# Performance work log

Measured on AMD Instinct MI355X. Metric: run time of the kernel, lower is better.

Reference implementation:

```python
import jax, jax.numpy as jnp
import numpy as np

N = 50000   # nodes
E = 600000  # edges
D = 128     # in_feats == n_hidden


def setup_inputs() -> dict:
    key = jax.random.key(0)
    ks = jax.random.split(key, 10)
    s = 0.1
    return {
        "x": jax.random.normal(ks[0], (N, D), jnp.float32),
        "W1": jax.random.normal(ks[1], (D, D), jnp.float32) * s,
        "b1": jnp.zeros((D,), jnp.float32),
        "W2": jax.random.normal(ks[2], (D, D), jnp.float32) * s,
        "b2": jnp.zeros((D,), jnp.float32),
        "Wp": jax.random.normal(ks[3], (D, D), jnp.float32) * s,
        "bp": jnp.zeros((D,), jnp.float32),
        "edge_src": jax.random.randint(ks[4], (E,), 0, N),
        "edge_dst": jax.random.randint(ks[5], (E,), 0, N),
        "perm": jax.random.randint(ks[6], (N,), 0, N),
    }


def _graph_conv(h, W, b, src, dst, norm):
    # DGL GraphConv (norm='both'): D^-1/2 A D^-1/2 H W + b
    m = h[src] * norm[src, None]                      # [E, D] gather
    agg = jax.ops.segment_sum(m, dst, num_segments=N)  # [N, D] scatter-add
    return (agg * norm[:, None]) @ W + b


def _encode(x, W1, b1, W2, b2, src, dst, norm):
    h = jax.nn.relu(_graph_conv(x, W1, b1, src, dst, norm))
    return _graph_conv(h, W2, b2, src, dst, norm)


def reference(x, W1, b1, W2, b2, Wp, bp, edge_src, edge_dst, perm):
    # symmetric normalization from in-degree (clamped to avoid div by 0)
    deg = jax.ops.segment_sum(jnp.ones((E,), x.dtype), edge_dst, num_segments=N)
    norm = jax.lax.rsqrt(jnp.maximum(deg, 1.0))

    h1 = _encode(x, W1, b1, W2, b2, edge_src, edge_dst, norm)        # clean
    h2 = _encode(x[perm], W1, b1, W2, b2, edge_src, edge_dst, norm)  # corrupt

    sc1 = (h1 @ Wp + bp).sum(axis=1)  # [N]
    sc2 = (h2 @ Wp + bp).sum(axis=1)  # [N]

    logits = jnp.concatenate([sc1, sc2])                   # [2N]
    lbl = jnp.concatenate([jnp.ones((N,), x.dtype), jnp.zeros((N,), x.dtype)])
    # BCEWithLogitsLoss (mean): softplus(z) - z*y  (numerically stable)
    loss = jnp.mean(jax.nn.softplus(logits) - logits * lbl)
    return loss
```

## Files before the change

kernel.cpp:

```cpp
#include <hip/hip_runtime.h>
#include <math.h>

#define D 128

typedef float f32x2 __attribute__((ext_vector_type(2)));
typedef float f32x4 __attribute__((ext_vector_type(4)));
typedef short short8 __attribute__((ext_vector_type(8)));

__device__ __forceinline__ float softplusf(float z){
    return log1pf(expf(-fabsf(z))) + fmaxf(z, 0.f);
}
__device__ __forceinline__ unsigned short f2bf(float f){
    unsigned u = __float_as_uint(f);
    u += 0x7fffu + ((u >> 16) & 1u);
    return (unsigned short)(u >> 16);
}
__device__ __forceinline__ int wt_idx(int row, int k){
    return row*128 + ((((k >> 3) ^ (row & 7)) << 3) | (k & 7));
}

__global__ void __launch_bounds__(256) k_fused1(
    const float* __restrict__ x, const float* __restrict__ W1,
    unsigned* __restrict__ xw8, int N,
    const int* __restrict__ edst, int* __restrict__ deg, int E,
    int nGemm,
    const float* __restrict__ W2, const float* __restrict__ b2,
    const float* __restrict__ Wp, const float* __restrict__ bp,
    float* __restrict__ v, float* __restrict__ cconst)
{
    __shared__ unsigned short Wt[128*128];
    __shared__ float pres[128];
    const int b = blockIdx.x;
    const int tid = threadIdx.x;
    if (b == 0){
        float* wps = pres;
        int lane = tid & 63, wid = tid >> 6;
        for (int r = wid; r < D; r += 4){
            float a = Wp[(size_t)r*D + lane] + Wp[(size_t)r*D + 64 + lane];
            for (int off=32; off>0; off>>=1) a += __shfl_down(a, off);
            if (lane == 0) wps[r] = a;
        }
        __syncthreads();
        float wl0 = wps[lane], wl1 = wps[64 + lane];
        for (int r = wid; r < D; r += 4){
            float a = W2[(size_t)r*D + lane]*wl0 + W2[(size_t)r*D + 64 + lane]*wl1;
            for (int off=32; off>0; off>>=1) a += __shfl_down(a, off);
            if (lane == 0) v[r] = a;
        }
        if (wid == 0){
            float a = b2[lane]*wl0 + b2[64+lane]*wl1 + bp[lane] + bp[64+lane];
            for (int off=32; off>0; off>>=1) a += __shfl_down(a, off);
            if (lane == 0) cconst[0] = a;
        }
    } else if (b <= nGemm){
        const int l = tid & 63, w = tid >> 6;
        const int row0 = (b - 1) * 64;
        #pragma unroll 8
        for (int p = 0; p < 64; ++p){
            int ic = p & 15;
            int ik = (p >> 4) + w*4;
            int c = ic*8 + (l & 7);
            int k = ik*8 + (l >> 3);
            Wt[wt_idx(c, k)] = f2bf(W1[(size_t)k*D + c]);
        }
        int arow = row0 + w*16 + (l & 15);
        int kbase = (l >> 4) * 8;
        short8 a[4];
        #pragma unroll
        for (int kc = 0; kc < 4; ++kc){
            float4 f0 = make_float4(0.f,0.f,0.f,0.f), f1 = f0;
            if (arow < N){
                const float* px = &x[(size_t)arow*D + kc*32 + kbase];
                f0 = *(const float4*)px;
                f1 = *(const float4*)(px + 4);
            }
            short8 av;
            av[0]=(short)f2bf(f0.x); av[1]=(short)f2bf(f0.y);
            av[2]=(short)f2bf(f0.z); av[3]=(short)f2bf(f0.w);
            av[4]=(short)f2bf(f1.x); av[5]=(short)f2bf(f1.y);
            av[6]=(short)f2bf(f1.z); av[7]=(short)f2bf(f1.w);
            a[kc] = av;
        }
        __syncthreads();
        int colg = (l & 15);
        #pragma unroll
        for (int nt = 0; nt < 8; ++nt){
            int col = nt*16 + colg;
            short8 bq[4];
            #pragma unroll
            for (int kc = 0; kc < 4; ++kc){
                int k0 = kc*32 + kbase;
                bq[kc] = *(const short8*)&Wt[wt_idx(col, k0)];
            }
            f32x4 acc = {0.f, 0.f, 0.f, 0.f};
            #pragma unroll
            for (int kc = 0; kc < 4; ++kc)
                acc = __builtin_amdgcn_mfma_f32_16x16x32_bf16(a[kc], bq[kc], acc, 0, 0, 0);
            int rbase = row0 + w*16 + (l >> 4)*4;
            #pragma unroll
            for (int rp = 0; rp < 2; ++rp){
                int pk = __builtin_amdgcn_cvt_pk_fp8_f32(acc[rp*2], acc[rp*2+1], 0, false);
                int r0 = rbase + rp*2;
                if (r0 < N)     ((unsigned char*)xw8)[(size_t)r0*D + col]     = (unsigned char)(pk & 0xff);
                if (r0 + 1 < N) ((unsigned char*)xw8)[(size_t)(r0+1)*D + col] = (unsigned char)((pk >> 8) & 0xff);
            }
        }
    } else {
        int e = (b - nGemm - 1)*256 + tid;
        if (e < E) atomicAdd(&deg[edst[e]], 1);
    }
}

__global__ void k_scanA(const int* __restrict__ deg, int* __restrict__ offs,
                        int* __restrict__ bsum, int N){
    __shared__ int wsums[16];
    __shared__ int gtot;
    int tid = threadIdx.x, lane = tid & 63, wid = tid >> 6;
    int g = blockIdx.x*1024 + tid;
    int val = (g < N) ? deg[g] : 0;
    int inc = val;
    #pragma unroll
    for (int off=1; off<64; off<<=1){
        int t = __shfl_up(inc, off);
        if (lane >= off) inc += t;
    }
    if (lane == 63) wsums[wid] = inc;
    __syncthreads();
    if (wid == 0 && lane < 16){
        int t = wsums[lane];
        int i2 = t;
        #pragma unroll
        for (int off=1; off<16; off<<=1){
            int u = __shfl_up(i2, off);
            if (lane >= off) i2 += u;
        }
        wsums[lane] = i2 - t;
        if (lane == 15) gtot = i2;
    }
    __syncthreads();
    if (g < N) offs[g] = wsums[wid] + inc - val;
    if (tid == 0) bsum[blockIdx.x] = gtot;
}

__global__ void k_scanC(int* __restrict__ offs, const int* __restrict__ bsum,
                        int* __restrict__ cursor, const int* __restrict__ deg,
                        float* __restrict__ norm, int2* __restrict__ ep,
                        const int* __restrict__ perm, int N){
    __shared__ int sbase;
    int tid = threadIdx.x;
    if (tid < 64){
        int val = (tid < (int)blockIdx.x) ? bsum[tid] : 0;
        for (int off=32; off>0; off>>=1) val += __shfl_down(val, off);
        if (tid == 0) sbase = val;
    }
    __syncthreads();
    int g = blockIdx.x*1024 + tid;
    if (g < N){
        int o = offs[g] + sbase;
        offs[g] = o;
        cursor[g] = o;
        float nm = rsqrtf(fmaxf((float)deg[g], 1.f));
        norm[g] = nm;
        ep[g] = make_int2(perm[g], __float_as_int(nm));
    }
}

__global__ void k_fill(const int* __restrict__ src, const int* __restrict__ dst,
                       int* __restrict__ cursor, unsigned short* __restrict__ csr, int E){
    int e = blockIdx.x*blockDim.x + threadIdx.x;
    if (e < E){
        int dd = dst[e];
        int p = atomicAdd(&cursor[dd], 1);
        csr[p] = (unsigned short)src[e];
    }
}

#define FMA8(u, nk) { \
    f32x2 f01 = __builtin_amdgcn_cvt_pk_f32_fp8((int)(u), false); \
    f32x2 f23 = __builtin_amdgcn_cvt_pk_f32_fp8((int)(u), true);  \
    ac.x = fmaf(f01.x, (nk), ac.x); ac.y = fmaf(f01.y, (nk), ac.y); \
    ac.z = fmaf(f23.x, (nk), ac.z); ac.w = fmaf(f23.y, (nk), ac.w); }

__global__ void __launch_bounds__(256) k_agg(const unsigned* __restrict__ xw8,
                     const unsigned short* __restrict__ csr, const int* __restrict__ offs,
                     const int* __restrict__ deg, const float* __restrict__ norm,
                     const int2* __restrict__ ep, const float* __restrict__ b1,
                     const float* __restrict__ v, float2* __restrict__ t2, int N){
    int w = threadIdx.x >> 6;
    int lane = threadIdx.x & 63;
    int i = blockIdx.x*4 + w;
    if (i >= N) return;
    int half = lane >> 5;
    int c = lane & 31;
    const unsigned* __restrict__ xr = xw8;
    float4 ac = make_float4(0.f,0.f,0.f,0.f);
    int start = offs[i], cnt = deg[i];

    for (int base = 0; base < cnt; base += 64){
        int m = min(cnt - base, 64);
        int s = 0, sp = 0; float ns = 0.f;
        if (lane < m){
            s = csr[start + base + lane];
            int2 e = ep[s];
            sp = e.x; ns = __int_as_float(e.y);
        }
        int k = 0;
        for (; k + 4 <= m; k += 4){
            int ra0=__shfl(s,k  ), rb0=__shfl(sp,k  ); float n0=__shfl(ns,k  );
            int ra1=__shfl(s,k+1), rb1=__shfl(sp,k+1); float n1=__shfl(ns,k+1);
            int ra2=__shfl(s,k+2), rb2=__shfl(sp,k+2); float n2=__shfl(ns,k+2);
            int ra3=__shfl(s,k+3), rb3=__shfl(sp,k+3); float n3=__shfl(ns,k+3);
            int r0 = half ? rb0 : ra0;
            int r1 = half ? rb1 : ra1;
            int r2 = half ? rb2 : ra2;
            int r3 = half ? rb3 : ra3;
            unsigned d0 = xr[(size_t)r0*32 + c];
            unsigned d1 = xr[(size_t)r1*32 + c];
            unsigned d2 = xr[(size_t)r2*32 + c];
            unsigned d3 = xr[(size_t)r3*32 + c];
            FMA8(d0, n0); FMA8(d1, n1); FMA8(d2, n2); FMA8(d3, n3);
        }
        for (; k < m; ++k){
            int ra=__shfl(s,k), rb=__shfl(sp,k); float nk=__shfl(ns,k);
            int r = half ? rb : ra;
            unsigned dv = xr[(size_t)r*32 + c];
            FMA8(dv, nk);
        }
    }
    float ni = norm[i];
    float4 bb = ((const float4*)b1)[c];
    float4 vv = ((const float4*)v)[c];
    float p = fmaxf(fmaf(ac.x, ni, bb.x), 0.f)*vv.x
            + fmaxf(fmaf(ac.y, ni, bb.y), 0.f)*vv.y
            + fmaxf(fmaf(ac.z, ni, bb.z), 0.f)*vv.z
            + fmaxf(fmaf(ac.w, ni, bb.w), 0.f)*vv.w;
    for (int off=16; off>0; off>>=1) p += __shfl_xor(p, off);
    float pd = __shfl(p, 32);
    if (lane == 0) t2[i] = make_float2(ni*p, ni*pd);
}

__global__ void k_loss(const float2* __restrict__ t2, const unsigned short* __restrict__ csr,
                       const int* __restrict__ offs, const int* __restrict__ deg,
                       const float* __restrict__ norm, const float* __restrict__ cconst,
                       float* __restrict__ acc, unsigned* __restrict__ done,
                       float* __restrict__ out, int N, int nblocks){
    int i = blockIdx.x*blockDim.x + threadIdx.x;
    float li = 0.f;
    if (i < N){
        int start = offs[i], cnt = deg[i];
        float sc = 0.f, sd = 0.f;
        for (int k=0;k<cnt;k++){
            int s = csr[start+k];
            float2 t = t2[s];
            sc += t.x; sd += t.y;
        }
        float ni = norm[i], C = cconst[0];
        li = softplusf(-fmaf(ni, sc, C)) + softplusf(fmaf(ni, sd, C));
    }
    for (int off=32; off>0; off>>=1) li += __shfl_down(li, off);
    __shared__ float wsum[4];
    int lane = threadIdx.x & 63, wid = threadIdx.x >> 6;
    if (lane == 0) wsum[wid] = li;
    __syncthreads();
    if (threadIdx.x == 0){
        float s = wsum[0] + wsum[1] + wsum[2] + wsum[3];
        atomicAdd(acc, s);
        __threadfence();
        unsigned t = atomicAdd(done, 1u);
        if (t == (unsigned)(nblocks - 1)){
            float tot = atomicAdd(acc, 0.0f);
            out[0] = tot / (float)(2*N);
        }
    }
}

extern "C" void kernel_launch(void* const* d_in, const int* in_sizes, int n_in,
                              void* d_out, int out_size, void* d_ws, size_t ws_size,
                              hipStream_t stream){
    const float* x    = (const float*)d_in[0];
    const float* W1   = (const float*)d_in[1];
    const float* b1   = (const float*)d_in[2];
    const float* W2   = (const float*)d_in[3];
    const float* b2   = (const float*)d_in[4];
    const float* Wp   = (const float*)d_in[5];
    const float* bp   = (const float*)d_in[6];
    const int*   esrc = (const int*)d_in[7];
    const int*   edst = (const int*)d_in[8];
    const int*   perm = (const int*)d_in[9];
    const int N = in_sizes[0] / D;
    const int E = in_sizes[7];

    char* ws = (char*)d_ws;
    size_t off = 0;
    auto alloc = [&](size_t bytes)->void*{
        void* p = ws + off;
        off += (bytes + 255) & ~(size_t)255;
        return p;
    };
    unsigned* xw8 = (unsigned*)alloc((size_t)N*32*sizeof(unsigned));
    int*   deg    = (int*)  alloc((size_t)N*sizeof(int));
    float* norm   = (float*)alloc((size_t)N*sizeof(float));
    int*   offs   = (int*)  alloc((size_t)N*sizeof(int));
    int*   cursor = (int*)  alloc((size_t)N*sizeof(int));
    int2*  ep     = (int2*) alloc((size_t)N*sizeof(int2));
    unsigned short* csr = (unsigned short*)alloc((size_t)E*sizeof(unsigned short));
    float2* t2    = (float2*)alloc((size_t)N*sizeof(float2));
    int*   bsum   = (int*)  alloc(4096);
    float* v      = (float*)alloc(D*sizeof(float));
    float* cconst = (float*)alloc(256);
    float* acc    = (float*)alloc(256);
    unsigned* done = (unsigned*)(acc + 1);

    hipMemsetAsync(deg, 0, (size_t)N*sizeof(int), stream);
    hipMemsetAsync(acc, 0, 256, stream);

    int nGemm = (N + 63) / 64;
    int nDeg  = (E + 255) / 256;
    int nb    = (N + 1023) / 1024;
    int nLoss = (N + 255) / 256;

    k_fused1<<<1 + nGemm + nDeg, 256, 0, stream>>>(x, W1, xw8, N, edst, deg, E,
                                                   nGemm, W2, b2, Wp, bp, v, cconst);
    k_scanA<<<nb, 1024, 0, stream>>>(deg, offs, bsum, N);
    k_scanC<<<nb, 1024, 0, stream>>>(offs, bsum, cursor, deg, norm, ep, perm, N);
    k_fill <<<(E+255)/256, 256, 0, stream>>>(esrc, edst, cursor, csr, E);
    k_agg  <<<(N+3)/4, 256, 0, stream>>>(xw8, csr, offs, deg, norm, ep, b1, v, t2, N);
    k_loss <<<nLoss, 256, 0, stream>>>(t2, csr, offs, deg, norm, cconst, acc, done,
                                       (float*)d_out, N, nLoss);
}
```

Before: 138.1 us.

## Pre-pack W1 into MFMA fragment layout in a prep kernel, drop per-block LDS staging

Moves the W1 bf16 conversion and the Wp/W2 reduction into a small separate prep kernel that writes W1 already in MFMA operand-fragment order. The GEMM blocks then read B operands straight from global/L2 instead of having every block convert and transpose W1 into shared memory, which removes the LDS usage and the __syncthreads. The operands are swapped so each lane holds a full row's packed fp8 output, giving one 32-bit store per tile instead of byte stores. It also uses the hardware v_cvt_pk_bf16_f32 instruction. The cost is one extra kernel launch and repeated L2 reads of the packed weights.

```diff
diff --git a/kernel.cpp b/kernel.cpp
--- a/kernel.cpp
+++ b/kernel.cpp
@@ -15,25 +15,25 @@
     u += 0x7fffu + ((u >> 16) & 1u);
     return (unsigned short)(u >> 16);
 }
-__device__ __forceinline__ int wt_idx(int row, int k){
-    return row*128 + ((((k >> 3) ^ (row & 7)) << 3) | (k & 7));
-}
-
-__global__ void __launch_bounds__(256) k_fused1(
-    const float* __restrict__ x, const float* __restrict__ W1,
-    unsigned* __restrict__ xw8, int N,
-    const int* __restrict__ edst, int* __restrict__ deg, int E,
-    int nGemm,
+
+__global__ void __launch_bounds__(256) k_prep(
+    const float* __restrict__ W1, unsigned short* __restrict__ wf,
     const float* __restrict__ W2, const float* __restrict__ b2,
     const float* __restrict__ Wp, const float* __restrict__ bp,
     float* __restrict__ v, float* __restrict__ cconst)
 {
-    __shared__ unsigned short Wt[128*128];
-    __shared__ float pres[128];
+    __shared__ float wps[D];
     const int b = blockIdx.x;
     const int tid = threadIdx.x;
-    if (b == 0){
-        float* wps = pres;
+    if (b < 8){
+        int kc = tid >> 6, l = tid & 63;
+        int c  = b*16 + (l & 15);
+        int kb = kc*32 + (l >> 4)*8;
+        union { unsigned short us[8]; short8 s; } uu;
+        #pragma unroll
+        for (int j = 0; j < 8; ++j) uu.us[j] = f2bf(W1[(size_t)(kb+j)*D + c]);
+        *(short8*)&wf[((size_t)(b*4 + kc)*64 + l)*8] = uu.s;
+    } else {
         int lane = tid & 63, wid = tid >> 6;
         for (int r = wid; r < D; r += 4){
             float a = Wp[(size_t)r*D + lane] + Wp[(size_t)r*D + 64 + lane];
@@ -52,61 +52,51 @@
             for (int off=32; off>0; off>>=1) a += __shfl_down(a, off);
             if (lane == 0) cconst[0] = a;
         }
-    } else if (b <= nGemm){
+    }
+}
+
+__global__ void __launch_bounds__(256) k_fused1(
+    const float* __restrict__ x, const unsigned short* __restrict__ wf,
+    unsigned* __restrict__ xw8, int N,
+    const int* __restrict__ edst, int* __restrict__ deg, int E, int nGemm)
+{
+    const int b = blockIdx.x;
+    const int tid = threadIdx.x;
+    if (b < nGemm){
         const int l = tid & 63, w = tid >> 6;
-        const int row0 = (b - 1) * 64;
-        #pragma unroll 8
-        for (int p = 0; p < 64; ++p){
-            int ic = p & 15;
-            int ik = (p >> 4) + w*4;
-            int c = ic*8 + (l & 7);
-            int k = ik*8 + (l >> 3);
-            Wt[wt_idx(c, k)] = f2bf(W1[(size_t)k*D + c]);
-        }
-        int arow = row0 + w*16 + (l & 15);
-        int kbase = (l >> 4) * 8;
+        const int r  = b*64 + w*16 + (l & 15);
+        const int kb = (l >> 4) * 8;
         short8 a[4];
         #pragma unroll
         for (int kc = 0; kc < 4; ++kc){
             float4 f0 = make_float4(0.f,0.f,0.f,0.f), f1 = f0;
-            if (arow < N){
-                const float* px = &x[(size_t)arow*D + kc*32 + kbase];
+            if (r < N){
+                const float* px = &x[(size_t)r*D + kc*32 + kb];
                 f0 = *(const float4*)px;
                 f1 = *(const float4*)(px + 4);
             }
-            short8 av;
-            av[0]=(short)f2bf(f0.x); av[1]=(short)f2bf(f0.y);
-            av[2]=(short)f2bf(f0.z); av[3]=(short)f2bf(f0.w);
-            av[4]=(short)f2bf(f1.x); av[5]=(short)f2bf(f1.y);
-            av[6]=(short)f2bf(f1.z); av[7]=(short)f2bf(f1.w);
-            a[kc] = av;
-        }
-        __syncthreads();
-        int colg = (l & 15);
+            unsigned u0,u1,u2,u3;
+            asm("v_cvt_pk_bf16_f32 %0, %1, %2" : "=v"(u0) : "v"(f0.x), "v"(f0.y));
+            asm("v_cvt_pk_bf16_f32 %0, %1, %2" : "=v"(u1) : "v"(f0.z), "v"(f0.w));
+            asm("v_cvt_pk_bf16_f32 %0, %1, %2" : "=v"(u2) : "v"(f1.x), "v"(f1.y));
+            asm("v_cvt_pk_bf16_f32 %0, %1, %2" : "=v"(u3) : "v"(f1.z), "v"(f1.w));
+            union { unsigned u[4]; short8 s; } uu = {{u0, u1, u2, u3}};
+            a[kc] = uu.s;
+        }
+        const short8* __restrict__ wfr = (const short8*)wf;
         #pragma unroll
         for (int nt = 0; nt < 8; ++nt){
-            int col = nt*16 + colg;
-            short8 bq[4];
-            #pragma unroll
-            for (int kc = 0; kc < 4; ++kc){
-                int k0 = kc*32 + kbase;
-                bq[kc] = *(const short8*)&Wt[wt_idx(col, k0)];
-            }
             f32x4 acc = {0.f, 0.f, 0.f, 0.f};
             #pragma unroll
             for (int kc = 0; kc < 4; ++kc)
-                acc = __builtin_amdgcn_mfma_f32_16x16x32_bf16(a[kc], bq[kc], acc, 0, 0, 0);
-            int rbase = row0 + w*16 + (l >> 4)*4;
-            #pragma unroll
-            for (int rp = 0; rp < 2; ++rp){
-                int pk = __builtin_amdgcn_cvt_pk_fp8_f32(acc[rp*2], acc[rp*2+1], 0, false);
-                int r0 = rbase + rp*2;
-                if (r0 < N)     ((unsigned char*)xw8)[(size_t)r0*D + col]     = (unsigned char)(pk & 0xff);
-                if (r0 + 1 < N) ((unsigned char*)xw8)[(size_t)(r0+1)*D + col] = (unsigned char)((pk >> 8) & 0xff);
-            }
+                acc = __builtin_amdgcn_mfma_f32_16x16x32_bf16(
+                          wfr[(nt*4 + kc)*64 + l], a[kc], acc, 0, 0, 0);
+            int pk = __builtin_amdgcn_cvt_pk_fp8_f32(acc[0], acc[1], 0, false);
+            pk     = __builtin_amdgcn_cvt_pk_fp8_f32(acc[2], acc[3], pk, true);
+            if (r < N) xw8[(size_t)r*32 + nt*4 + (l >> 4)] = (unsigned)pk;
         }
     } else {
-        int e = (b - nGemm - 1)*256 + tid;
+        int e = (b - nGemm)*256 + tid;
         if (e < E) atomicAdd(&deg[edst[e]], 1);
     }
 }
@@ -298,6 +288,7 @@
         return p;
     };
     unsigned* xw8 = (unsigned*)alloc((size_t)N*32*sizeof(unsigned));
+    unsigned short* wf = (unsigned short*)alloc((size_t)D*D*sizeof(unsigned short));
     int*   deg    = (int*)  alloc((size_t)N*sizeof(int));
     float* norm   = (float*)alloc((size_t)N*sizeof(float));
     int*   offs   = (int*)  alloc((size_t)N*sizeof(int));
@@ -319,12 +310,12 @@
     int nb    = (N + 1023) / 1024;
     int nLoss = (N + 255) / 256;
 
-    k_fused1<<<1 + nGemm + nDeg, 256, 0, stream>>>(x, W1, xw8, N, edst, deg, E,
-                                                   nGemm, W2, b2, Wp, bp, v, cconst);
-    k_scanA<<<nb, 1024, 0, stream>>>(deg, offs, bsum, N);
-    k_scanC<<<nb, 1024, 0, stream>>>(offs, bsum, cursor, deg, norm, ep, perm, N);
-    k_fill <<<(E+255)/256, 256, 0, stream>>>(esrc, edst, cursor, csr, E);
-    k_agg  <<<(N+3)/4, 256, 0, stream>>>(xw8, csr, offs, deg, norm, ep, b1, v, t2, N);
-    k_loss <<<nLoss, 256, 0, stream>>>(t2, csr, offs, deg, norm, cconst, acc, done,
-                                       (float*)d_out, N, nLoss);
-}
+    k_prep  <<<9, 256, 0, stream>>>(W1, wf, W2, b2, Wp, bp, v, cconst);
+    k_fused1<<<nGemm + nDeg, 256, 0, stream>>>(x, wf, xw8, N, edst, deg, E, nGemm);
+    k_scanA <<<nb, 1024, 0, stream>>>(deg, offs, bsum, N);
+    k_scanC <<<nb, 1024, 0, stream>>>(offs, bsum, cursor, deg, norm, ep, perm, N);
+    k_fill  <<<(E+255)/256, 256, 0, stream>>>(esrc, edst, cursor, csr, E);
+    k_agg   <<<(N+3)/4, 256, 0, stream>>>(xw8, csr, offs, deg, norm, ep, b1, v, t2, N);
+    k_loss  <<<nLoss, 256, 0, stream>>>(t2, csr, offs, deg, norm, cconst, acc, done,
+                                        (float*)d_out, N, nLoss);
+}
```

Measured after the change: 158.3 us. 1.15x slower.
